# Performance work log

Measured on AMD Instinct MI355X. Metric: run time of the kernel, lower is better.

The kernel has to match this reference:

```python
import jax, jax.numpy as jnp
import numpy as np

INPUT_DIMS = 512
OUTPUT_DIMS = 512
GRID_SIZE = 8


def setup_inputs() -> dict:
    key = jax.random.key(0)
    k_x, k_w = jax.random.split(key)
    x = jax.random.normal(k_x, (4, 2048, INPUT_DIMS), dtype=jnp.float32)
    scale = 1.0 / (np.sqrt(INPUT_DIMS) * np.sqrt(GRID_SIZE))
    fouriercoeffs = jax.random.normal(
        k_w, (2, OUTPUT_DIMS, INPUT_DIMS, GRID_SIZE), dtype=jnp.float32) * scale
    bias = jnp.zeros((1, OUTPUT_DIMS), dtype=jnp.float32)
    return {"x": x, "fouriercoeffs": fouriercoeffs, "bias": bias}


def reference(x, fouriercoeffs, bias):
    out_shape = x.shape[:-1] + (OUTPUT_DIMS,)
    xf = x.reshape(-1, INPUT_DIMS)  # [N, I]
    k = jnp.arange(1, GRID_SIZE + 1, dtype=x.dtype)  # [G]
    arg = xf[:, :, None] * k  # [N, I, G]
    # contract cos/sin features against coeffs: two batched GEMMs
    y = jnp.einsum('nig,oig->no', jnp.cos(arg), fouriercoeffs[0])
    y = y + jnp.einsum('nig,oig->no', jnp.sin(arg), fouriercoeffs[1])
    y = y + bias
    return y.reshape(out_shape)
```

## Files before the change

### kernel.cpp

```cpp
#include <hip/hip_runtime.h>
#include <hip/hip_bf16.h>


typedef __attribute__((ext_vector_type(8))) short s16x8;
typedef __attribute__((ext_vector_type(4))) int   i32x4;
typedef __attribute__((ext_vector_type(4))) float f32x4;

#define NROWS 8192
#define IDIM  512
#define ODIM  512
#define KDIM  8192

static __device__ __forceinline__ short f2bf(float f) {
    union { float f; unsigned u; } v; v.f = f;
    unsigned r = v.u + 0x7fffu + ((v.u >> 16) & 1u);
    return (short)(r >> 16);
}

static __device__ __forceinline__ int pkbf(float c, float s) {
    union { __hip_bfloat162 h; int i; } u;
    u.h = __float22bfloat162_rn(make_float2(c, s));
    return u.i;
}

__global__ __launch_bounds__(256) void fkan_prep(const float* __restrict__ cf,
                                                 short* __restrict__ Wb) {
    const int o = blockIdx.x;
    const int tid = threadIdx.x;
#pragma unroll
    for (int rep = 0; rep < 2; ++rep) {
        const int i = tid + rep * 256;
        const float* c0 = cf + (o * 512 + i) * 8;
        const float* c1 = cf + ((512 + o) * 512 + i) * 8;
        float4 a0 = *(const float4*)c0;
        float4 a1 = *(const float4*)(c0 + 4);
        float4 b0 = *(const float4*)c1;
        float4 b1 = *(const float4*)(c1 + 4);
        s16x8 lo, hi;
        lo[0] = f2bf(a0.x); lo[1] = f2bf(b0.x);
        lo[2] = f2bf(a0.y); lo[3] = f2bf(b0.y);
        lo[4] = f2bf(a0.z); lo[5] = f2bf(b0.z);
        lo[6] = f2bf(a0.w); lo[7] = f2bf(b0.w);
        hi[0] = f2bf(a1.x); hi[1] = f2bf(b1.x);
        hi[2] = f2bf(a1.y); hi[3] = f2bf(b1.y);
        hi[4] = f2bf(a1.z); hi[5] = f2bf(b1.z);
        hi[6] = f2bf(a1.w); hi[7] = f2bf(b1.w);
        *(s16x8*)(Wb + o * KDIM + i * 16)     = lo;
        *(s16x8*)(Wb + o * KDIM + i * 16 + 8) = hi;
    }
}

template <int KSPLIT>
__global__ __launch_bounds__(256, 2) void fkan_gemm(const float* __restrict__ x,
                                                    const short* __restrict__ Wb,
                                                    const float* __restrict__ bias,
                                                    float* __restrict__ outp) {
    __shared__ short As[2][128 * 64];
    __shared__ short Bs[2][128 * 64];

    const int bid = blockIdx.x;
    int bn, kc, bm;
    if (KSPLIT == 2) {
        const int xcd = bid & 7;
        bn = xcd & 3; kc = xcd >> 2; bm = bid >> 3;
    } else {
        const int xcd = bid & 7, idx = bid >> 3;
        bn = xcd & 3; kc = 0; bm = idx + (xcd >> 2) * 32;
    }
    const int n0 = bm * 128, o0 = bn * 128;
    const int NKT = 128 / KSPLIT;
    const int i0 = kc * (512 / KSPLIT);
    const int kbase = i0 * 16;

    const int tid = threadIdx.x;
    const int wid = tid >> 6, lane = tid & 63;
    const int lrow = lane & 15, lk = lane >> 4;
    const int wr = wid >> 1, wc = wid & 1;

    f32x4 acc[4][4];
#pragma unroll
    for (int a = 0; a < 4; ++a)
#pragma unroll
        for (int b = 0; b < 4; ++b) {
            f32x4 z = {0.f, 0.f, 0.f, 0.f};
            acc[a][b] = z;
        }

    const int nl = tid >> 1, isel = tid & 1;
    const float* xrow = x + (n0 + nl) * 512 + i0 + isel * 2;

    auto stage = [&](int t, int nb, float2 xvv) {
#pragma unroll
        for (int w = 0; w < 4; ++w) {
            const int chunk = w * 256 + tid;
            const int r = chunk >> 3, pc = chunk & 7;
            const int lc = pc ^ (r & 7);
            const short* src = Wb + (o0 + r) * KDIM + kbase + t * 64 + lc * 8;
            short* ldst = &Bs[nb][w * 2048 + wid * 512];
            __builtin_amdgcn_global_load_lds(
                (const __attribute__((address_space(1))) void*)src,
                (__attribute__((address_space(3))) void*)ldst, 16, 0, 0);
        }
#pragma unroll
        for (int ii = 0; ii < 2; ++ii) {
            const float xx = ii ? xvv.y : xvv.x;
            float s1, c1;
            __sincosf(xx, &s1, &c1);
            float c = c1, s = s1;
            i32x4 lo, hi;
#pragma unroll
            for (int g = 0; g < 8; ++g) {
                const int p = pkbf(c, s);
                if (g < 4) lo[g] = p; else hi[g - 4] = p;
                const float t1 = s * s1, t2 = c * s1;
                const float cn = __builtin_fmaf(c, c1, -t1);
                s = __builtin_fmaf(s, c1, t2);
                c = cn;
            }
            const int il = isel * 2 + ii;
            const int cb0 = il * 2;
            *(i32x4*)&As[nb][nl * 64 + ((cb0 ^ (nl & 7))) * 8]       = lo;
            *(i32x4*)&As[nb][nl * 64 + (((cb0 + 1) ^ (nl & 7))) * 8] = hi;
        }
    };

    float2 xv = *(const float2*)xrow;
    stage(0, 0, xv);
    xv = *(const float2*)(xrow + 4);
    __syncthreads();

    for (int kt = 0; kt < NKT; ++kt) {
        const int cur = kt & 1;
        const short* Ab = As[cur];
        const short* Bb = Bs[cur];

        s16x8 af[2][4], bfr[2][4];
#pragma unroll
        for (int ksub = 0; ksub < 2; ++ksub) {
#pragma unroll
            for (int mf = 0; mf < 4; ++mf) {
                const int row = wr * 64 + mf * 16 + lrow;
                af[ksub][mf] = *(const s16x8*)&Ab[row * 64 + ((ksub * 4 + lk) ^ (row & 7)) * 8];
            }
#pragma unroll
            for (int nf = 0; nf < 4; ++nf) {
                const int row = wc * 64 + nf * 16 + lrow;
                bfr[ksub][nf] = *(const s16x8*)&Bb[row * 64 + ((ksub * 4 + lk) ^ (row & 7)) * 8];
            }
        }

        if (kt + 1 < NKT) {
            stage(kt + 1, cur ^ 1, xv);
            if (kt + 2 < NKT) xv = *(const float2*)(xrow + (kt + 2) * 4);
        }

#pragma unroll
        for (int ksub = 0; ksub < 2; ++ksub)
#pragma unroll
            for (int mf = 0; mf < 4; ++mf)
#pragma unroll
                for (int nf = 0; nf < 4; ++nf)
                    acc[mf][nf] = __builtin_amdgcn_mfma_f32_16x16x32_bf16(
                        af[ksub][mf], bfr[ksub][nf], acc[mf][nf], 0, 0, 0);

        __syncthreads();
    }

    float* dst = (KSPLIT == 2) ? (outp + (size_t)kc * (NROWS * ODIM)) : outp;
#pragma unroll
    for (int nf = 0; nf < 4; ++nf) {
        const int oc = o0 + wc * 64 + nf * 16 + lrow;
        const float bv = (KSPLIT == 1) ? bias[oc] : 0.f;
#pragma unroll
        for (int mf = 0; mf < 4; ++mf) {
            const f32x4 v = acc[mf][nf];
            const int rbase = n0 + wr * 64 + mf * 16 + lk * 4;
#pragma unroll
            for (int j = 0; j < 4; ++j)
                dst[(rbase + j) * 512 + oc] = v[j] + bv;
        }
    }
}

__global__ __launch_bounds__(256) void fkan_combine(const float* __restrict__ P,
                                                    const float* __restrict__ bias,
                                                    float* __restrict__ out) {
    const int total = NROWS * ODIM / 4;
    for (int idx = blockIdx.x * 256 + threadIdx.x; idx < total;
         idx += gridDim.x * 256) {
        float4 a = ((const float4*)P)[idx];
        float4 b = ((const float4*)P)[total + idx];
        float4 c = ((const float4*)bias)[idx & 127];
        float4 r;
        r.x = a.x + b.x + c.x;
        r.y = a.y + b.y + c.y;
        r.z = a.z + b.z + c.z;
        r.w = a.w + b.w + c.w;
        ((float4*)out)[idx] = r;
    }
}

extern "C" void kernel_launch(void* const* d_in, const int* in_sizes, int n_in,
                              void* d_out, int out_size, void* d_ws, size_t ws_size,
                              hipStream_t stream) {
    const float* x    = (const float*)d_in[0];
    const float* cf   = (const float*)d_in[1];
    const float* bias = (const float*)d_in[2];
    float* out = (float*)d_out;

    const size_t partial_bytes = (size_t)2 * NROWS * ODIM * 4;
    const size_t wb_bytes = (size_t)ODIM * KDIM * 2;

    if (ws_size >= partial_bytes + wb_bytes) {
        float* P  = (float*)d_ws;
        short* Wb = (short*)((char*)d_ws + partial_bytes);
        fkan_prep<<<512, 256, 0, stream>>>(cf, Wb);
        fkan_gemm<2><<<512, 256, 0, stream>>>(x, Wb, bias, P);
        fkan_combine<<<1024, 256, 0, stream>>>(P, bias, out);
    } else {
        short* Wb = (short*)d_ws;
        fkan_prep<<<512, 256, 0, stream>>>(cf, Wb);
        fkan_gemm<1><<<256, 256, 0, stream>>>(x, Wb, bias, out);
    }
}
```

Measured before the change: 100.7 us.

## Load B fragments directly from global memory instead of staging through LDS

Removes the LDS double buffer for the weight tile. Each wave now reads its B MFMA fragments straight from global memory (L2) every k-step, which frees LDS for occupancy and drops the async LDS copies. The cost is that each B element is fetched redundantly by both wave rows, and the global loads sit on the critical path with no prefetch ahead of the MFMAs.

```diff
diff --git a/kernel.cpp b/kernel.cpp
--- a/kernel.cpp
+++ b/kernel.cpp
@@ -56,7 +56,6 @@
                                                     const float* __restrict__ bias,
                                                     float* __restrict__ outp) {
     __shared__ short As[2][128 * 64];
-    __shared__ short Bs[2][128 * 64];
 
     const int bid = blockIdx.x;
     int bn, kc, bm;
@@ -86,21 +85,12 @@
             acc[a][b] = z;
         }
 
+    const short* bptr = Wb + (o0 + wc * 64 + lrow) * KDIM + kbase + lk * 8;
+
     const int nl = tid >> 1, isel = tid & 1;
     const float* xrow = x + (n0 + nl) * 512 + i0 + isel * 2;
 
-    auto stage = [&](int t, int nb, float2 xvv) {
-#pragma unroll
-        for (int w = 0; w < 4; ++w) {
-            const int chunk = w * 256 + tid;
-            const int r = chunk >> 3, pc = chunk & 7;
-            const int lc = pc ^ (r & 7);
-            const short* src = Wb + (o0 + r) * KDIM + kbase + t * 64 + lc * 8;
-            short* ldst = &Bs[nb][w * 2048 + wid * 512];
-            __builtin_amdgcn_global_load_lds(
-                (const __attribute__((address_space(1))) void*)src,
-                (__attribute__((address_space(3))) void*)ldst, 16, 0, 0);
-        }
+    auto stageA = [&](int nb, float2 xvv) {
 #pragma unroll
         for (int ii = 0; ii < 2; ++ii) {
             const float xx = ii ? xvv.y : xvv.x;
@@ -125,32 +115,35 @@
     };
 
     float2 xv = *(const float2*)xrow;
-    stage(0, 0, xv);
+    stageA(0, xv);
     xv = *(const float2*)(xrow + 4);
     __syncthreads();
 
     for (int kt = 0; kt < NKT; ++kt) {
         const int cur = kt & 1;
         const short* Ab = As[cur];
-        const short* Bb = Bs[cur];
-
-        s16x8 af[2][4], bfr[2][4];
-#pragma unroll
-        for (int ksub = 0; ksub < 2; ++ksub) {
+
+        s16x8 bfr[2][4];
+        {
+            const short* bk = bptr + kt * 64;
+#pragma unroll
+            for (int ksub = 0; ksub < 2; ++ksub)
+#pragma unroll
+                for (int nf = 0; nf < 4; ++nf)
+                    bfr[ksub][nf] = *(const s16x8*)(bk + ksub * 32 + nf * (16 * KDIM));
+        }
+
+        s16x8 af[2][4];
+#pragma unroll
+        for (int ksub = 0; ksub < 2; ++ksub)
 #pragma unroll
             for (int mf = 0; mf < 4; ++mf) {
                 const int row = wr * 64 + mf * 16 + lrow;
                 af[ksub][mf] = *(const s16x8*)&Ab[row * 64 + ((ksub * 4 + lk) ^ (row & 7)) * 8];
             }
-#pragma unroll
-            for (int nf = 0; nf < 4; ++nf) {
-                const int row = wc * 64 + nf * 16 + lrow;
-                bfr[ksub][nf] = *(const s16x8*)&Bb[row * 64 + ((ksub * 4 + lk) ^ (row & 7)) * 8];
-            }
-        }
 
         if (kt + 1 < NKT) {
-            stage(kt + 1, cur ^ 1, xv);
+            stageA(cur ^ 1, xv);
             if (kt + 2 < NKT) xv = *(const float2*)(xrow + (kt + 2) * 4);
         }
 
```

After: 146.6 us. 1.46x slower.

## Store split-K partials in bf16 and raise wave priority around MFMA loop

Applied to the files above, without the earlier changes.

The split-K GEMM now writes its two partial sums as bf16 instead of fp32, halving partial write traffic and the combine kernel's reads. The combine kernel reads 8 bf16 values per thread and runs with more blocks. s_setprio is raised around the MFMA block so waves issuing matrix ops get scheduling priority. Rounding partials to bf16 before summing adds precision loss to the output.

```diff
diff --git a/kernel.cpp b/kernel.cpp
--- a/kernel.cpp
+++ b/kernel.cpp
@@ -15,6 +15,12 @@
     union { float f; unsigned u; } v; v.f = f;
     unsigned r = v.u + 0x7fffu + ((v.u >> 16) & 1u);
     return (short)(r >> 16);
+}
+
+static __device__ __forceinline__ float bf2f(short h) {
+    union { unsigned u; float f; } v;
+    v.u = ((unsigned)(unsigned short)h) << 16;
+    return v.f;
 }
 
 static __device__ __forceinline__ int pkbf(float c, float s) {
@@ -54,7 +60,7 @@
 __global__ __launch_bounds__(256, 2) void fkan_gemm(const float* __restrict__ x,
                                                     const short* __restrict__ Wb,
                                                     const float* __restrict__ bias,
-                                                    float* __restrict__ outp) {
+                                                    void* __restrict__ outp) {
     __shared__ short As[2][128 * 64];
     __shared__ short Bs[2][128 * 64];
 
@@ -154,6 +160,7 @@
             if (kt + 2 < NKT) xv = *(const float2*)(xrow + (kt + 2) * 4);
         }
 
+        __builtin_amdgcn_s_setprio(1);
 #pragma unroll
         for (int ksub = 0; ksub < 2; ++ksub)
 #pragma unroll
@@ -162,41 +169,65 @@
                 for (int nf = 0; nf < 4; ++nf)
                     acc[mf][nf] = __builtin_amdgcn_mfma_f32_16x16x32_bf16(
                         af[ksub][mf], bfr[ksub][nf], acc[mf][nf], 0, 0, 0);
+        __builtin_amdgcn_s_setprio(0);
 
         __syncthreads();
     }
 
-    float* dst = (KSPLIT == 2) ? (outp + (size_t)kc * (NROWS * ODIM)) : outp;
-#pragma unroll
-    for (int nf = 0; nf < 4; ++nf) {
-        const int oc = o0 + wc * 64 + nf * 16 + lrow;
-        const float bv = (KSPLIT == 1) ? bias[oc] : 0.f;
-#pragma unroll
-        for (int mf = 0; mf < 4; ++mf) {
-            const f32x4 v = acc[mf][nf];
-            const int rbase = n0 + wr * 64 + mf * 16 + lk * 4;
-#pragma unroll
-            for (int j = 0; j < 4; ++j)
-                dst[(rbase + j) * 512 + oc] = v[j] + bv;
-        }
-    }
-}
-
-__global__ __launch_bounds__(256) void fkan_combine(const float* __restrict__ P,
+    if (KSPLIT == 2) {
+        unsigned short* dst = (unsigned short*)outp + (size_t)kc * (NROWS * ODIM);
+#pragma unroll
+        for (int nf = 0; nf < 4; ++nf) {
+            const int oc = o0 + wc * 64 + nf * 16 + lrow;
+#pragma unroll
+            for (int mf = 0; mf < 4; ++mf) {
+                const f32x4 v = acc[mf][nf];
+                const int rbase = n0 + wr * 64 + mf * 16 + lk * 4;
+#pragma unroll
+                for (int j = 0; j < 4; ++j)
+                    dst[(size_t)(rbase + j) * 512 + oc] = (unsigned short)f2bf(v[j]);
+            }
+        }
+    } else {
+        float* dst = (float*)outp;
+#pragma unroll
+        for (int nf = 0; nf < 4; ++nf) {
+            const int oc = o0 + wc * 64 + nf * 16 + lrow;
+            const float bv = bias[oc];
+#pragma unroll
+            for (int mf = 0; mf < 4; ++mf) {
+                const f32x4 v = acc[mf][nf];
+                const int rbase = n0 + wr * 64 + mf * 16 + lk * 4;
+#pragma unroll
+                for (int j = 0; j < 4; ++j)
+                    dst[(size_t)(rbase + j) * 512 + oc] = v[j] + bv;
+            }
+        }
+    }
+}
+
+__global__ __launch_bounds__(256) void fkan_combine(const short* __restrict__ P,
                                                     const float* __restrict__ bias,
                                                     float* __restrict__ out) {
-    const int total = NROWS * ODIM / 4;
-    for (int idx = blockIdx.x * 256 + threadIdx.x; idx < total;
-         idx += gridDim.x * 256) {
-        float4 a = ((const float4*)P)[idx];
-        float4 b = ((const float4*)P)[total + idx];
-        float4 c = ((const float4*)bias)[idx & 127];
-        float4 r;
-        r.x = a.x + b.x + c.x;
-        r.y = a.y + b.y + c.y;
-        r.z = a.z + b.z + c.z;
-        r.w = a.w + b.w + c.w;
-        ((float4*)out)[idx] = r;
+    const int total = NROWS * ODIM;
+    const int stride = gridDim.x * 256 * 8;
+    for (int e = (blockIdx.x * 256 + threadIdx.x) * 8; e < total; e += stride) {
+        s16x8 a = *(const s16x8*)(P + e);
+        s16x8 b = *(const s16x8*)(P + total + e);
+        const int col = e & 511;
+        float4 c0 = *(const float4*)(bias + col);
+        float4 c1 = *(const float4*)(bias + col + 4);
+        float4 r0, r1;
+        r0.x = bf2f(a[0]) + bf2f(b[0]) + c0.x;
+        r0.y = bf2f(a[1]) + bf2f(b[1]) + c0.y;
+        r0.z = bf2f(a[2]) + bf2f(b[2]) + c0.z;
+        r0.w = bf2f(a[3]) + bf2f(b[3]) + c0.w;
+        r1.x = bf2f(a[4]) + bf2f(b[4]) + c1.x;
+        r1.y = bf2f(a[5]) + bf2f(b[5]) + c1.y;
+        r1.z = bf2f(a[6]) + bf2f(b[6]) + c1.z;
+        r1.w = bf2f(a[7]) + bf2f(b[7]) + c1.w;
+        *(float4*)(out + e)     = r0;
+        *(float4*)(out + e + 4) = r1;
     }
 }
 
@@ -208,18 +239,18 @@
     const float* bias = (const float*)d_in[2];
     float* out = (float*)d_out;
 
-    const size_t partial_bytes = (size_t)2 * NROWS * ODIM * 4;
+    const size_t partial_bytes = (size_t)2 * NROWS * ODIM * 2;
     const size_t wb_bytes = (size_t)ODIM * KDIM * 2;
 
     if (ws_size >= partial_bytes + wb_bytes) {
-        float* P  = (float*)d_ws;
+        short* P  = (short*)d_ws;
         short* Wb = (short*)((char*)d_ws + partial_bytes);
         fkan_prep<<<512, 256, 0, stream>>>(cf, Wb);
-        fkan_gemm<2><<<512, 256, 0, stream>>>(x, Wb, bias, P);
-        fkan_combine<<<1024, 256, 0, stream>>>(P, bias, out);
+        fkan_gemm<2><<<512, 256, 0, stream>>>(x, Wb, bias, (void*)P);
+        fkan_combine<<<2048, 256, 0, stream>>>(P, bias, out);
     } else {
         short* Wb = (short*)d_ws;
         fkan_prep<<<512, 256, 0, stream>>>(cf, Wb);
-        fkan_gemm<1><<<256, 256, 0, stream>>>(x, Wb, bias, out);
-    }
-}
+        fkan_gemm<1><<<256, 256, 0, stream>>>(x, Wb, bias, (void*)out);
+    }
+}
```

Result: no change. 102.3 us (+1.6%).
